# Optimization experiments

Hardware: AMD Instinct MI355X
Metric: run time of the kernel (lower is better)

Reference implementation:

```python
import jax, jax.numpy as jnp
import numpy as np

B, C, DET, T = 16, 1, 512, 180  # batch, channels, detector size (= image side, circle=True), n angles


def setup_inputs() -> dict:
    key = jax.random.key(0)
    x = jax.random.normal(key, (B, C, DET, T), dtype=jnp.float32)  # sinogram [B,C,det,theta]
    return {"x": x}


def _ramp_filter(x):
    """skimage-style ramp (Ram-Lak) filter along detector axis (axis=2)."""
    det = x.shape[2]
    size = max(64, int(2 ** np.ceil(np.log2(2 * det))))  # zero-padded FFT length
    n = np.concatenate([np.arange(1, size // 2 + 1, 2), np.arange(size // 2 - 1, 0, -2)])
    f = np.zeros(size, dtype=np.float64)
    f[0] = 0.25
    f[1::2] = -1.0 / (np.pi * n) ** 2
    fourier = (2.0 * np.real(np.fft.fft(f))).astype(np.float32)  # [size]
    xp = jnp.pad(x, ((0, 0), (0, 0), (0, size - det), (0, 0)))
    proj = jnp.fft.fft(xp, axis=2) * fourier[None, None, :, None]
    return jnp.real(jnp.fft.ifft(proj, axis=2))[:, :, :det, :].astype(x.dtype)


def _forward(x):
    b, c, det, n_theta = x.shape
    xf = _ramp_filter(x)
    # align_corners=False unit grid over the image (circle=True -> grid side == det)
    u = ((2.0 * jnp.arange(det, dtype=x.dtype) + 1.0) / det - 1.0)
    yg = u[:, None]  # [det,1] (meshgrid 'ij': Y varies over rows)
    xg = u[None, :]  # [1,det]
    rad = jnp.arange(n_theta, dtype=x.dtype) * jnp.asarray(np.pi / 180.0, x.dtype)
    cos_t, sin_t = jnp.cos(rad), jnp.sin(rad)

    # Note: the grid X coord theta_x[i]=(2i+1)/T-1 maps (align_corners=False) to pixel
    # index exactly i, so the width-axis bilinear interp reduces to taking angle column i.
    def body(reco, inp):
        i, c_, s_ = inp
        col = jax.lax.dynamic_index_in_dim(xf, i, axis=3, keepdims=False)  # [B,C,det]
        t = xg * c_ - yg * s_                      # [det,det] rotated coordinate
        iy = ((t + 1.0) * det - 1.0) / 2.0         # grid_sample align_corners=False
        i0f = jnp.floor(iy)
        w1 = iy - i0f
        w0 = 1.0 - w1
        i0 = i0f.astype(jnp.int32)
        i1 = i0 + 1
        m0 = ((i0 >= 0) & (i0 < det)).astype(xf.dtype)  # zeros padding
        m1 = ((i1 >= 0) & (i1 < det)).astype(xf.dtype)
        g0 = jnp.take(col, jnp.clip(i0, 0, det - 1), axis=2)  # [B,C,det,det]
        g1 = jnp.take(col, jnp.clip(i1, 0, det - 1), axis=2)
        return reco + (w0 * m0) * g0 + (w1 * m1) * g1, None

    reco0 = jnp.zeros((b, c, det, det), xf.dtype)
    reco, _ = jax.lax.scan(body, reco0, (jnp.arange(n_theta), cos_t, sin_t))

    # reconstruction circle mask (scikit=False -> radius^2 <= 1 - 1/in_size)
    mask = (xg ** 2 + yg ** 2) <= (1.0 - 1.0 / det)
    reco = jnp.where(mask[None, None], reco, jnp.zeros((), reco.dtype))
    return reco * jnp.asarray(np.pi / (2.0 * n_theta), reco.dtype)


def reference(x):
    return _forward(x)
```

## Files before the change

### kernel.cpp

```cpp
#include <hip/hip_runtime.h>
#include <math.h>

#define DET 512
#define NB  16
#define NT  180
#define PI_D 3.14159265358979323846
#define NPAIR 89
#define PADQ 108
#define NGP  45
#define PKI_ROW 1536
#define NOFF 101
#define NMRG 6
#define NBX  108

#define TT_OFF   8192
#define XF0_OFF  (TT_OFF + 512*512*2)
#define XF90_OFF (XF0_OFF + 32768)
#define PK_OFF   (XF90_OFF + 32768)

typedef _Float16 half8  __attribute__((ext_vector_type(8)));
typedef _Float16 half4v __attribute__((ext_vector_type(4)));
typedef _Float16 half2v __attribute__((ext_vector_type(2)));
typedef float    float4v __attribute__((ext_vector_type(4)));

__device__ inline void fmix_lo(float& acc, float w, unsigned int pk) {
  asm("v_fma_mix_f32 %0, %1, %2, %0 op_sel_hi:[0,1,0]"
      : "+v"(acc) : "v"(w), "v"(pk));
}
__device__ inline void fmix_hi(float& acc, float w, unsigned int pk) {
  asm("v_fma_mix_f32 %0, %1, %2, %0 op_sel:[0,1,0] op_sel_hi:[0,1,0]"
      : "+v"(acc) : "v"(w), "v"(pk));
}

__global__ __launch_bounds__(256) void filter_kernel(const float* __restrict__ x,
                                                     char* __restrict__ wsb) {
  __shared__ _Float16 xs_h[16][512];
  __shared__ _Float16 xs_l[16][512];
  __shared__ float xfs[16][65];
  __shared__ _Float16 wls[8][1032];
  unsigned int* pkg = (unsigned int*)(wsb + PK_OFF);

  int tid = threadIdx.x;
  int p = blockIdx.x, b = blockIdx.y;
  int dt0 = blockIdx.z * 2;

  {
    int k0 = tid * 4;
    const float CSC = (float)(-2048.0 / (PI_D * PI_D));
#pragma unroll
    for (int r = 0; r < 8; r++) {
      half4v v;
#pragma unroll
      for (int j = 0; j < 4; j++) {
        int delta = 511 - (k0 + j) - r;
        float wv;
        if (delta == 0) wv = 512.0f;
        else if (delta & 1) wv = CSC / (float)(delta * delta);
        else wv = 0.0f;
        v[j] = (_Float16)wv;
      }
      *(half4v*)&wls[r][k0] = v;
    }
  }

  int m = tid & 15, kp = tid >> 4;
  int tS;
  if (p < 11) tS = (m < 8) ? (8 * p + 1 + m) : (164 - 8 * p + m);
  else        tS = (m == 0) ? 89 : ((m == 1) ? 91 : ((m == 3) ? 90 : 0));
  const float* xb = x + (size_t)b * DET * NT + tS;
#pragma unroll 8
  for (int pass = 0; pass < 16; pass++) {
    int k = pass * 32 + kp * 2;
    int c = k >> 3, h = k & 7;
    int phys = (((c ^ (m & 7)) << 3) | h);
    float v0 = xb[(size_t)k * NT];
    float v1 = xb[(size_t)(k + 1) * NT];
    _Float16 h0 = (_Float16)v0, h1 = (_Float16)v1;
    half2v hh = {h0, h1};
    half2v ll = {(_Float16)(v0 - (float)h0), (_Float16)(v1 - (float)h1)};
    *(half2v*)&xs_h[m][phys] = hh;
    *(half2v*)&xs_l[m][phys] = ll;
  }
  __syncthreads();

  int nprb = (p < 11) ? 8 : 1;
  int tpb0 = (p < 11) ? 8 * p : 88;
  if (blockIdx.z == 0) {
    int idx = (tid < 108) ? tid : (620 + (tid - 108));
    uint2 z2; z2.x = 0u; z2.y = 0u;
    for (int pr = 0; pr < nprb; pr++) {
      int tq = (p < 11) ? (tpb0 + pr) : 88;
      int gp = (tq <= 44) ? tq : 88 - tq;
      *(uint2*)&pkg[((size_t)b * NGP + gp) * PKI_ROW + 2 * idx] = z2;
    }
  }

  int lane = tid & 63, wv = tid >> 6;
  int mm = lane & 15, q = lane >> 4;
  const _Float16* arh = &xs_h[mm][0];
  const _Float16* arl = &xs_l[mm][0];
  int e = mm & 7;
  int mp = tid >> 5, cc = (tid & 31) * 2;
  int rT = (p < 11) ? mp : 0;
  int rU = (p < 11) ? (15 - mp) : 1;
  int tpp = (p < 11) ? (8 * p + mp) : 88;
  bool dopack = (p < 11) || (mp == 0);
  int gp_  = (tpp <= 44) ? tpp : 88 - tpp;
  int slot = (tpp <= 44) ? 0 : 1;

  for (int dti = 0; dti < 2; dti++) {
    int dt = dt0 + dti;
    int dw = dt * 64 + wv * 16 + mm;
    int sdw = 511 - dw;
    const _Float16* thl = &wls[sdw & 7][sdw & ~7];
    float4v acc0 = {0.f, 0.f, 0.f, 0.f};
    float4v acc1 = {0.f, 0.f, 0.f, 0.f};
#pragma unroll 4
    for (int kc = 0; kc < 512; kc += 32) {
      int ph = ((((kc >> 3) + q) ^ e) << 3);
      half8 Ah = *(const half8*)&arh[ph];
      half8 Al = *(const half8*)&arl[ph];
      half8 Bh = *(const half8*)&thl[kc + q * 8];
      acc0 = __builtin_amdgcn_mfma_f32_16x16x32_f16(Ah, Bh, acc0, 0, 0, 0);
      acc1 = __builtin_amdgcn_mfma_f32_16x16x32_f16(Al, Bh, acc1, 0, 0, 0);
    }
    if (dti > 0) __syncthreads();
#pragma unroll
    for (int i = 0; i < 4; i++)
      xfs[q * 4 + i][wv * 16 + mm] = (acc0[i] + acc1[i]) * 0.0009765625f;
    __syncthreads();
    if (dopack) {
      float ft0 = xfs[rT][cc], ft1 = xfs[rT][cc + 1];
      float fu0 = xfs[rU][cc], fu1 = xfs[rU][cc + 1];
      auto p0 = __builtin_amdgcn_cvt_pkrtz(ft0, fu0);
      auto p1 = __builtin_amdgcn_cvt_pkrtz(ft1, fu1);
      unsigned int w0, w1;
      __builtin_memcpy(&w0, &p0, 4);
      __builtin_memcpy(&w1, &p1, 4);
      unsigned int* row = pkg + ((size_t)b * NGP + gp_) * PKI_ROW;
      int en = PADQ + dt * 64 + cc;
      row[2 * en + slot]     = w0;
      row[2 * en + 2 + slot] = w1;
      if (tpp == 44) {
        row[2 * en + 1] = w0;
        row[2 * en + 3] = w1;
      }
    }
    if (p == 11 && tid < 64) {
      float* f0  = (float*)(wsb + XF0_OFF)  + (size_t)b * DET;
      float* f90 = (float*)(wsb + XF90_OFF) + (size_t)b * DET;
      f0[dt * 64 + tid]  = xfs[2][tid];
      f90[dt * 64 + tid] = xfs[3][tid];
    }
  }
}


#define PROCESS(c_, s_, SW)                                                    \
  {                                                                            \
    float inner = fmaf(-(s_), q_, 363.5f);                                     \
    float iyA = fmaf( (c_), p_, inner);                                        \
    float iyB = fmaf(-(c_), p_, inner);                                        \
    int   iA = (int)iyA;  float wA = __builtin_amdgcn_fractf(iyA);             \
    int   iB = (int)iyB;  float wB = __builtin_amdgcn_fractf(iyB);             \
    float vA = 1.f - wA, vB = 1.f - wB;                                        \
    uint4 rA, rB, rMA, rMB;                                                    \
    __builtin_memcpy(&rA,  &colI[2 * iA], 16);                                 \
    __builtin_memcpy(&rB,  &colI[2 * iB], 16);                                 \
    __builtin_memcpy(&rMA, &colI[2 * (726 - iA)], 16);                         \
    __builtin_memcpy(&rMB, &colI[2 * (726 - iB)], 16);                         \
    unsigned tA0 = SW ? rA.y : rA.x,  tA1 = SW ? rA.w : rA.z;                  \
    unsigned uA0 = SW ? rA.x : rA.y,  uA1 = SW ? rA.z : rA.w;                  \
    unsigned tB0 = SW ? rB.y : rB.x,  tB1 = SW ? rB.w : rB.z;                  \
    unsigned uB0 = SW ? rB.x : rB.y,  uB1 = SW ? rB.z : rB.w;                  \
    unsigned tMA0 = SW ? rMA.y : rMA.x,  tMA1 = SW ? rMA.w : rMA.z;            \
    unsigned uMA0 = SW ? rMA.x : rMA.y,  uMA1 = SW ? rMA.z : rMA.w;            \
    unsigned tMB0 = SW ? rMB.y : rMB.x,  tMB1 = SW ? rMB.w : rMB.z;            \
    unsigned uMB0 = SW ? rMB.x : rMB.y,  uMB1 = SW ? rMB.z : rMB.w;            \
    fmix_lo(A1, vA, tA0);  fmix_lo(A1, wA, tA1);                               \
    fmix_hi(A1, vB, tB0);  fmix_hi(A1, wB, tB1);                               \
    fmix_lo(A2, vB, tB0);  fmix_lo(A2, wB, tB1);                               \
    fmix_hi(A2, vA, tA0);  fmix_hi(A2, wA, tA1);                               \
    fmix_lo(A3, wA, tMA0); fmix_lo(A3, vA, tMA1);                              \
    fmix_hi(A3, wB, tMB0); fmix_hi(A3, vB, tMB1);                              \
    fmix_lo(A4, wB, tMB0); fmix_lo(A4, vB, tMB1);                              \
    fmix_hi(A4, wA, tMA0); fmix_hi(A4, vA, tMA1);                              \
    fmix_lo(B1, wA, uMA0); fmix_lo(B1, vA, uMA1);                              \
    fmix_hi(B1, vB, uB0);  fmix_hi(B1, wB, uB1);                               \
    fmix_lo(B2, wB, uMB0); fmix_lo(B2, vB, uMB1);                              \
    fmix_hi(B2, vA, uA0);  fmix_hi(B2, wA, uA1);                               \
    fmix_lo(B3, vA, uA0);  fmix_lo(B3, wA, uA1);                               \
    fmix_hi(B3, wB, uMB0); fmix_hi(B3, vB, uMB1);                              \
    fmix_lo(B4, vB, uB0);  fmix_lo(B4, wB, uB1);                               \
    fmix_hi(B4, wA, uMA0); fmix_hi(B4, vA, uMA1);                              \
  }

#define PROCESSP(c_, s_, SW, pp, qq, AA1, AA2, AA3, AA4)                       \
  {                                                                            \
    float inner = fmaf(-(s_), (qq), 363.5f);                                   \
    float iyA = fmaf( (c_), (pp), inner);                                      \
    float iyB = fmaf(-(c_), (pp), inner);                                      \
    int   iA = (int)iyA;  float wA = __builtin_amdgcn_fractf(iyA);             \
    int   iB = (int)iyB;  float wB = __builtin_amdgcn_fractf(iyB);             \
    float vA = 1.f - wA, vB = 1.f - wB;                                        \
    uint4 rA, rB, rMA, rMB;                                                    \
    __builtin_memcpy(&rA,  &colI[2 * iA], 16);                                 \
    __builtin_memcpy(&rB,  &colI[2 * iB], 16);                                 \
    __builtin_memcpy(&rMA, &colI[2 * (726 - iA)], 16);                         \
    __builtin_memcpy(&rMB, &colI[2 * (726 - iB)], 16);                         \
    unsigned tA0 = SW ? rA.y : rA.x,  tA1 = SW ? rA.w : rA.z;                  \
    unsigned tB0 = SW ? rB.y : rB.x,  tB1 = SW ? rB.w : rB.z;                  \
    unsigned tMA0 = SW ? rMA.y : rMA.x,  tMA1 = SW ? rMA.w : rMA.z;            \
    unsigned tMB0 = SW ? rMB.y : rMB.x,  tMB1 = SW ? rMB.w : rMB.z;            \
    fmix_lo(AA1, vA, tA0);  fmix_lo(AA1, wA, tA1);                             \
    fmix_hi(AA1, vB, tB0);  fmix_hi(AA1, wB, tB1);                             \
    fmix_lo(AA2, vB, tB0);  fmix_lo(AA2, wB, tB1);                             \
    fmix_hi(AA2, vA, tA0);  fmix_hi(AA2, wA, tA1);                             \
    fmix_lo(AA3, wA, tMA0); fmix_lo(AA3, vA, tMA1);                            \
    fmix_hi(AA3, wB, tMB0); fmix_hi(AA3, vB, tMB1);                            \
    fmix_lo(AA4, wB, tMB0); fmix_lo(AA4, vB, tMB1);                            \
    fmix_hi(AA4, wA, tMA0); fmix_hi(AA4, vA, tMA1);                            \
  }

__global__ __launch_bounds__(256, 8) void backproj_kernel(
    const char* __restrict__ wsb, float* __restrict__ out) {
  __shared__ unsigned int pk[2][PKI_ROW];
  __shared__ float2 trigs[48];
  int tid = threadIdx.x;
  int b   = blockIdx.y;
  int bx  = blockIdx.x;
  int lx = tid & 15, ly = tid >> 4;
  float* ob = out + (size_t)b * DET * DET;
  int w = tid >> 6, l = tid & 63;

  if (bx == NOFF + NMRG) {
    const int LDEAD[10] = {10,8,6,5,4,3,2,2,1,1};
    for (int a = 0; a < 10; a++)
      for (int bt = 0; bt < LDEAD[a]; bt++) {
        int X1 = 16*a + lx, X2 = 511 - X1;
        int Y1 = 16*bt + ly, Y2 = 511 - Y1;
        ob[(size_t)Y1*DET + X1] = 0.f;
        ob[(size_t)Y1*DET + X2] = 0.f;
        ob[(size_t)Y2*DET + X1] = 0.f;
        ob[(size_t)Y2*DET + X2] = 0.f;
      }
    return;
  }

  if (tid < NGP) {
    float th = (float)(tid + 1) * (float)(PI_D / 180.0);
    float2 cs; cs.x = cosf(th); cs.y = sinf(th);
    trigs[tid] = cs;
  }

  const unsigned int* pkg = (const unsigned int*)(wsb + PK_OFF) + (size_t)b * NGP * PKI_ROW;

  auto stage_group = [&](int g, int par) {
    {
      const unsigned int* src = pkg + (size_t)g * PKI_ROW + w * 256 + l * 4;
      char* dst = (char*)&pk[par][0] + w * 1024;
      __builtin_amdgcn_global_load_lds(
          (const __attribute__((address_space(1))) unsigned int*)src,
          (__attribute__((address_space(3))) unsigned int*)dst, 16, 0, 0);
    }
    if (w < 2) {
      const unsigned int* src = pkg + (size_t)g * PKI_ROW + (w + 4) * 256 + l * 4;
      char* dst = (char*)&pk[par][0] + (w + 4) * 1024;
      __builtin_amdgcn_global_load_lds(
          (const __attribute__((address_space(1))) unsigned int*)src,
          (__attribute__((address_space(3))) unsigned int*)dst, 16, 0, 0);
    }
  };

  const float* f0  = (const float*)(wsb + XF0_OFF)  + (size_t)b * DET;
  const float* f90 = (const float*)(wsb + XF90_OFF) + (size_t)b * DET;
  const float SC = (float)(PI_D / 360.0);

  if (bx >= NOFF) {
    int d = bx - NOFF;
    int a1 = 4 + 2 * d, a2 = 5 + 2 * d;
    float p1_ = (float)(16 * a1 + lx) - 255.5f, q1_ = (float)(16 * a1 + ly) - 255.5f;
    float p2_ = (float)(16 * a2 + lx) - 255.5f, q2_ = (float)(16 * a2 + ly) - 255.5f;
    int mk1 = 481 - 32 * a1, mn1 = 505 - 32 * a1 - 8 * w;
    int mk2 = 481 - 32 * a2, mn2 = 505 - 32 * a2 - 8 * w;
    bool wl1 = (mk1 * mk1 + mn1 * mn1 <= 261632);
    bool wl2 = (mk2 * mk2 + mn2 * mn2 <= 261632);

    float A1=0.f, A2=0.f, A3=0.f, A4=0.f;
    float C1=0.f, C2=0.f, C3=0.f, C4=0.f;

    stage_group(0, 0);
    __syncthreads();
    for (int g = 0; g < NGP; g++) {
      if (g + 1 < NGP) stage_group(g + 1, (g + 1) & 1);
      float2 cs = trigs[g];
      const unsigned int* colI = &pk[g & 1][0];
      if (wl1) {
        PROCESSP(cs.x, cs.y, 0, p1_, q1_, A1, A2, A3, A4);
        if (g != 44) PROCESSP(cs.y, cs.x, 1, p1_, q1_, A1, A2, A3, A4);
      }
      if (wl2) {
        PROCESSP(cs.x, cs.y, 0, p2_, q2_, C1, C2, C3, C4);
        if (g != 44) PROCESSP(cs.y, cs.x, 1, p2_, q2_, C1, C2, C3, C4);
      }
      __syncthreads();
    }
#pragma unroll
    for (int t = 0; t < 2; t++) {
      int a = t ? a2 : a1;
      int X1 = 16 * a + lx, X2 = 511 - X1;
      int Y1 = 16 * a + ly, Y2 = 511 - Y1;
      int kx = 2 * X1 - 511, ky = 2 * Y1 - 511;
      bool in = (kx * kx + ky * ky) <= 261632;
      float g0x1 = f0[X1], g0x2 = f0[X2];
      float g90y1 = f90[Y1], g90y2 = f90[Y2];
      float P1 = (t ? C1 : A1) + g0x1 + g90y2;
      float P2 = (t ? C2 : A2) + g0x2 + g90y2;
      float P3 = (t ? C3 : A3) + g0x2 + g90y1;
      float P4 = (t ? C4 : A4) + g0x1 + g90y1;
      ob[(size_t)Y1 * DET + X1] = in ? P1 * SC : 0.f;
      ob[(size_t)Y1 * DET + X2] = in ? P2 * SC : 0.f;
      ob[(size_t)Y2 * DET + X2] = in ? P3 * SC : 0.f;
      ob[(size_t)Y2 * DET + X1] = in ? P4 * SC : 0.f;
    }
    return;
  }

  int a = (bx>=6)+(bx>=14)+(bx>=24)+(bx>=35)+(bx>=46)+(bx>=56)+(bx>=65)
        + (bx>=73)+(bx>=80)+(bx>=86)+(bx>=91)+(bx>=95)+(bx>=98)+(bx>=100);
  int Sa, bs;
  if (a < 8) { Sa = (int)((0x41382E23180E0600ULL >> (8*a)) & 0xFF);
               bs = (int)((0x080706050506080AULL >> (8*a)) & 0xFF); }
  else       { Sa = (int)((0x0064625F5B565049ULL >> (8*(a-8))) & 0xFF);
               bs = (int)((0x000F0E0D0C0B0A09ULL >> (8*(a-8))) & 0xFF); }
  int bt = bx - Sa + bs;
  int tx = 16*a, ty = 16*bt;

  int X1 = tx + lx, X2 = 511 - X1;
  int Y1 = ty + ly, Y2 = 511 - Y1;
  float p_ = (float)X1 - 255.5f;
  float q_ = (float)Y1 - 255.5f;

  int mkx = 481 - 32*a;
  int mky = 505 - 32*bt - 8*w;
  bool wlive = (mkx*mkx + mky*mky <= 261632);

  float A1=0.f, A2=0.f, A3=0.f, A4=0.f;
  float B1=0.f, B2=0.f, B3=0.f, B4=0.f;

  stage_group(0, 0);
  __syncthreads();

  for (int g = 0; g < NGP; g++) {
    if (g + 1 < NGP) stage_group(g + 1, (g + 1) & 1);
    float2 cs = trigs[g];
    const unsigned int* colI = &pk[g & 1][0];
    if (wlive) {
      PROCESS(cs.x, cs.y, 0);
      if (g != 44) PROCESS(cs.y, cs.x, 1);
    }
    __syncthreads();
  }

  int kx = 2*X1 - 511, ky = 2*Y1 - 511;
  bool in = (kx*kx + ky*ky) <= 261632;

  float g0x1 = f0[X1], g0x2 = f0[X2];
  float g90y1 = f90[Y1], g90y2 = f90[Y2];
  float P1 = A1 + g0x1 + g90y2;
  float P2 = A2 + g0x2 + g90y2;
  float P3 = A3 + g0x2 + g90y1;
  float P4 = A4 + g0x1 + g90y1;
  ob[(size_t)Y1*DET + X1] = in ? P1*SC : 0.f;
  ob[(size_t)Y1*DET + X2] = in ? P2*SC : 0.f;
  ob[(size_t)Y2*DET + X2] = in ? P3*SC : 0.f;
  ob[(size_t)Y2*DET + X1] = in ? P4*SC : 0.f;

  {
    float g0y1 = f0[Y1], g0y2 = f0[Y2];
    float g90x1 = f90[X1], g90x2 = f90[X2];
    float Q1 = B1 + g0y1 + g90x2;
    float Q2 = B2 + g0y1 + g90x1;
    float Q3 = B3 + g0y2 + g90x1;
    float Q4 = B4 + g0y2 + g90x2;
    Q1 = in ? Q1*SC : 0.f;
    Q2 = in ? Q2*SC : 0.f;
    Q3 = in ? Q3*SC : 0.f;
    Q4 = in ? Q4*SC : 0.f;
    __syncthreads();
    float* qs = (float*)&pk[0][0];
    qs[(0*16 + lx)*17 + ly] = Q1;
    qs[(1*16 + lx)*17 + ly] = Q2;
    qs[(2*16 + lx)*17 + ly] = Q3;
    qs[(3*16 + lx)*17 + ly] = Q4;
    __syncthreads();
    float o1 = qs[(0*16 + ly)*17 + lx];
    float o2 = qs[(1*16 + ly)*17 + lx];
    float o3 = qs[(2*16 + ly)*17 + lx];
    float o4 = qs[(3*16 + ly)*17 + lx];
    int r1 = tx + ly, r2 = 511 - r1;
    int c1 = ty + lx, c2 = 511 - c1;
    ob[(size_t)r1*DET + c1] = o1;
    ob[(size_t)r2*DET + c1] = o2;
    ob[(size_t)r2*DET + c2] = o3;
    ob[(size_t)r1*DET + c2] = o4;
  }
}

extern "C" void kernel_launch(void* const* d_in, const int* in_sizes, int n_in,
                              void* d_out, int out_size, void* d_ws, size_t ws_size,
                              hipStream_t stream) {
  (void)in_sizes; (void)n_in; (void)out_size; (void)ws_size;
  const float* x = (const float*)d_in[0];
  float* out = (float*)d_out;
  char*  wsb = (char*)d_ws;

  filter_kernel<<<dim3(12, 16, 4), 256, 0, stream>>>(x, wsb);
  backproj_kernel<<<dim3(NBX, NB), 256, 0, stream>>>(wsb, out);
}
```

Before: 139.2 us.

## Repack filtered projections as 16-byte entries and use fdot2 interpolation

The packed sinogram layout changes so each 16-byte entry already holds both neighbouring detector samples (i0 and i0+1) for the two paired angles. The backprojection can then fetch one uint4 per lookup and do each bilinear interpolation with a single packed-half fdot2 instead of two fma_mix ops. Weights are packed into half2 via cvt_pkrtz, which lowers weight precision to fp16. The change also doubles the LDS staging buffer, lowers the launch-bounds occupancy hint from 8 to 6, and flattens the grid with batch-interleaved block indexing. The filter kernel now writes duplicated half values with scattered 2-byte stores, which adds write traffic.

```diff
diff --git a/kernel.cpp b/kernel.cpp
--- a/kernel.cpp
+++ b/kernel.cpp
@@ -8,7 +8,8 @@
 #define NPAIR 89
 #define PADQ 108
 #define NGP  45
-#define PKI_ROW 1536
+#define NENT 768
+#define ROWB 12288
 #define NOFF 101
 #define NMRG 6
 #define NBX  108
@@ -23,13 +24,13 @@
 typedef _Float16 half2v __attribute__((ext_vector_type(2)));
 typedef float    float4v __attribute__((ext_vector_type(4)));
 
-__device__ inline void fmix_lo(float& acc, float w, unsigned int pk) {
-  asm("v_fma_mix_f32 %0, %1, %2, %0 op_sel_hi:[0,1,0]"
-      : "+v"(acc) : "v"(w), "v"(pk));
+__device__ inline half2v H2(unsigned u) { half2v h; __builtin_memcpy(&h, &u, 4); return h; }
+__device__ inline half2v pkrtz(float a, float b) {
+  auto r = __builtin_amdgcn_cvt_pkrtz(a, b);
+  half2v h; __builtin_memcpy(&h, &r, 4); return h;
 }
-__device__ inline void fmix_hi(float& acc, float w, unsigned int pk) {
-  asm("v_fma_mix_f32 %0, %1, %2, %0 op_sel:[0,1,0] op_sel_hi:[0,1,0]"
-      : "+v"(acc) : "v"(w), "v"(pk));
+__device__ inline float fdot2f(half2v a, half2v b, float c) {
+  return __builtin_amdgcn_fdot2(a, b, c, false);
 }
 
 __global__ __launch_bounds__(256) void filter_kernel(const float* __restrict__ x,
@@ -38,7 +39,7 @@
   __shared__ _Float16 xs_l[16][512];
   __shared__ float xfs[16][65];
   __shared__ _Float16 wls[8][1032];
-  unsigned int* pkg = (unsigned int*)(wsb + PK_OFF);
+  char* pkb = wsb + PK_OFF;
 
   int tid = threadIdx.x;
   int p = blockIdx.x, b = blockIdx.y;
@@ -86,12 +87,23 @@
   int nprb = (p < 11) ? 8 : 1;
   int tpb0 = (p < 11) ? 8 * p : 88;
   if (blockIdx.z == 0) {
-    int idx = (tid < 108) ? tid : (620 + (tid - 108));
-    uint2 z2; z2.x = 0u; z2.y = 0u;
     for (int pr = 0; pr < nprb; pr++) {
       int tq = (p < 11) ? (tpb0 + pr) : 88;
       int gp = (tq <= 44) ? tq : 88 - tq;
-      *(uint2*)&pkg[((size_t)b * NGP + gp) * PKI_ROW + 2 * idx] = z2;
+      char* base = pkb + ((size_t)b * NGP + gp) * ROWB;
+      if (tid < 107) {
+        uint4 z4 = {0u, 0u, 0u, 0u};
+        *(uint4*)(base + (size_t)tid * 16) = z4;
+      } else if (tid < 255) {
+        uint4 z4 = {0u, 0u, 0u, 0u};
+        *(uint4*)(base + (size_t)(620 + tid - 107) * 16) = z4;
+      } else {
+        unsigned short z = 0;
+        *(unsigned short*)(base + 107*16 + 0)  = z; *(unsigned short*)(base + 107*16 + 4)  = z;
+        *(unsigned short*)(base + 107*16 + 8)  = z; *(unsigned short*)(base + 107*16 + 12) = z;
+        *(unsigned short*)(base + 619*16 + 2)  = z; *(unsigned short*)(base + 619*16 + 6)  = z;
+        *(unsigned short*)(base + 619*16 + 10) = z; *(unsigned short*)(base + 619*16 + 14) = z;
+      }
     }
   }
 
@@ -106,7 +118,7 @@
   int tpp = (p < 11) ? (8 * p + mp) : 88;
   bool dopack = (p < 11) || (mp == 0);
   int gp_  = (tpp <= 44) ? tpp : 88 - tpp;
-  int slot = (tpp <= 44) ? 0 : 1;
+  int so   = (tpp <= 44) ? 0 : 8;
 
   for (int dti = 0; dti < 2; dti++) {
     int dt = dt0 + dti;
@@ -130,20 +142,23 @@
       xfs[q * 4 + i][wv * 16 + mm] = (acc0[i] + acc1[i]) * 0.0009765625f;
     __syncthreads();
     if (dopack) {
-      float ft0 = xfs[rT][cc], ft1 = xfs[rT][cc + 1];
-      float fu0 = xfs[rU][cc], fu1 = xfs[rU][cc + 1];
-      auto p0 = __builtin_amdgcn_cvt_pkrtz(ft0, fu0);
-      auto p1 = __builtin_amdgcn_cvt_pkrtz(ft1, fu1);
-      unsigned int w0, w1;
-      __builtin_memcpy(&w0, &p0, 4);
-      __builtin_memcpy(&w1, &p1, 4);
-      unsigned int* row = pkg + ((size_t)b * NGP + gp_) * PKI_ROW;
-      int en = PADQ + dt * 64 + cc;
-      row[2 * en + slot]     = w0;
-      row[2 * en + 2 + slot] = w1;
-      if (tpp == 44) {
-        row[2 * en + 1] = w0;
-        row[2 * en + 3] = w1;
+      char* base = pkb + ((size_t)b * NGP + gp_) * ROWB;
+#pragma unroll
+      for (int ci = 0; ci < 2; ci++) {
+        int c = cc + ci;
+        _Float16 ftc = (_Float16)xfs[rT][c];
+        _Float16 fuc = (_Float16)xfs[rU][c];
+        int en = PADQ + dt * 64 + c;
+        *(_Float16*)(base + (size_t)en * 16 + 0 + so)       = ftc;
+        *(_Float16*)(base + (size_t)(en - 1) * 16 + 2 + so) = ftc;
+        *(_Float16*)(base + (size_t)en * 16 + 4 + so)       = fuc;
+        *(_Float16*)(base + (size_t)(en - 1) * 16 + 6 + so) = fuc;
+        if (tpp == 44) {
+          *(_Float16*)(base + (size_t)en * 16 + 8)        = ftc;
+          *(_Float16*)(base + (size_t)(en - 1) * 16 + 10) = ftc;
+          *(_Float16*)(base + (size_t)en * 16 + 12)       = fuc;
+          *(_Float16*)(base + (size_t)(en - 1) * 16 + 14) = fuc;
+        }
       }
     }
     if (p == 11 && tid < 64) {
@@ -155,6 +170,9 @@
   }
 }
 
+#define XTRACT(nm, qq, SW)                                                     \
+  half2v Tft##nm = H2(SW ? qq.z : qq.x), Tfu##nm = H2(SW ? qq.w : qq.y);       \
+  half2v Uft##nm = H2(SW ? qq.x : qq.z), Ufu##nm = H2(SW ? qq.y : qq.w);
 
 #define PROCESS(c_, s_, SW)                                                    \
   {                                                                            \
@@ -163,77 +181,61 @@
     float iyB = fmaf(-(c_), p_, inner);                                        \
     int   iA = (int)iyA;  float wA = __builtin_amdgcn_fractf(iyA);             \
     int   iB = (int)iyB;  float wB = __builtin_amdgcn_fractf(iyB);             \
-    float vA = 1.f - wA, vB = 1.f - wB;                                        \
-    uint4 rA, rB, rMA, rMB;                                                    \
-    __builtin_memcpy(&rA,  &colI[2 * iA], 16);                                 \
-    __builtin_memcpy(&rB,  &colI[2 * iB], 16);                                 \
-    __builtin_memcpy(&rMA, &colI[2 * (726 - iA)], 16);                         \
-    __builtin_memcpy(&rMB, &colI[2 * (726 - iB)], 16);                         \
-    unsigned tA0 = SW ? rA.y : rA.x,  tA1 = SW ? rA.w : rA.z;                  \
-    unsigned uA0 = SW ? rA.x : rA.y,  uA1 = SW ? rA.z : rA.w;                  \
-    unsigned tB0 = SW ? rB.y : rB.x,  tB1 = SW ? rB.w : rB.z;                  \
-    unsigned uB0 = SW ? rB.x : rB.y,  uB1 = SW ? rB.z : rB.w;                  \
-    unsigned tMA0 = SW ? rMA.y : rMA.x,  tMA1 = SW ? rMA.w : rMA.z;            \
-    unsigned uMA0 = SW ? rMA.x : rMA.y,  uMA1 = SW ? rMA.z : rMA.w;            \
-    unsigned tMB0 = SW ? rMB.y : rMB.x,  tMB1 = SW ? rMB.w : rMB.z;            \
-    unsigned uMB0 = SW ? rMB.x : rMB.y,  uMB1 = SW ? rMB.z : rMB.w;            \
-    fmix_lo(A1, vA, tA0);  fmix_lo(A1, wA, tA1);                               \
-    fmix_hi(A1, vB, tB0);  fmix_hi(A1, wB, tB1);                               \
-    fmix_lo(A2, vB, tB0);  fmix_lo(A2, wB, tB1);                               \
-    fmix_hi(A2, vA, tA0);  fmix_hi(A2, wA, tA1);                               \
-    fmix_lo(A3, wA, tMA0); fmix_lo(A3, vA, tMA1);                              \
-    fmix_hi(A3, wB, tMB0); fmix_hi(A3, vB, tMB1);                              \
-    fmix_lo(A4, wB, tMB0); fmix_lo(A4, vB, tMB1);                              \
-    fmix_hi(A4, wA, tMA0); fmix_hi(A4, vA, tMA1);                              \
-    fmix_lo(B1, wA, uMA0); fmix_lo(B1, vA, uMA1);                              \
-    fmix_hi(B1, vB, uB0);  fmix_hi(B1, wB, uB1);                               \
-    fmix_lo(B2, wB, uMB0); fmix_lo(B2, vB, uMB1);                              \
-    fmix_hi(B2, vA, uA0);  fmix_hi(B2, wA, uA1);                               \
-    fmix_lo(B3, vA, uA0);  fmix_lo(B3, wA, uA1);                               \
-    fmix_hi(B3, wB, uMB0); fmix_hi(B3, vB, uMB1);                              \
-    fmix_lo(B4, vB, uB0);  fmix_lo(B4, wB, uB1);                               \
-    fmix_hi(B4, wA, uMA0); fmix_hi(B4, vA, uMA1);                              \
-  }
-
-#define PROCESSP(c_, s_, SW, pp, qq, AA1, AA2, AA3, AA4)                       \
+    half2v wpA = pkrtz(1.f - wA, wA);                                          \
+    half2v wpAr = pkrtz(wA, 1.f - wA);                                         \
+    half2v wpB = pkrtz(1.f - wB, wB);                                          \
+    half2v wpBr = pkrtz(wB, 1.f - wB);                                         \
+    uint4 qA = colI[iA], qB = colI[iB];                                        \
+    uint4 qMA = colI[726 - iA], qMB = colI[726 - iB];                          \
+    XTRACT(A, qA, SW)  XTRACT(B, qB, SW)                                       \
+    XTRACT(MA, qMA, SW) XTRACT(MB, qMB, SW)                                    \
+    A1 = fdot2f(wpA, TftA, A1);   A1 = fdot2f(wpB, TfuB, A1);                  \
+    A2 = fdot2f(wpB, TftB, A2);   A2 = fdot2f(wpA, TfuA, A2);                  \
+    A3 = fdot2f(wpAr, TftMA, A3); A3 = fdot2f(wpBr, TfuMB, A3);                \
+    A4 = fdot2f(wpBr, TftMB, A4); A4 = fdot2f(wpAr, TfuMA, A4);                \
+    B1 = fdot2f(wpAr, UftMA, B1); B1 = fdot2f(wpB, UfuB, B1);                  \
+    B2 = fdot2f(wpBr, UftMB, B2); B2 = fdot2f(wpA, UfuA, B2);                  \
+    B3 = fdot2f(wpA, UftA, B3);   B3 = fdot2f(wpBr, UfuMB, B3);                \
+    B4 = fdot2f(wpB, UftB, B4);   B4 = fdot2f(wpAr, UfuMA, B4);                \
+  }
+
+#define PROCESSP(c_, s_, SW, pp, qq_, AA1, AA2, AA3, AA4)                      \
   {                                                                            \
-    float inner = fmaf(-(s_), (qq), 363.5f);                                   \
+    float inner = fmaf(-(s_), (qq_), 363.5f);                                  \
     float iyA = fmaf( (c_), (pp), inner);                                      \
     float iyB = fmaf(-(c_), (pp), inner);                                      \
     int   iA = (int)iyA;  float wA = __builtin_amdgcn_fractf(iyA);             \
     int   iB = (int)iyB;  float wB = __builtin_amdgcn_fractf(iyB);             \
-    float vA = 1.f - wA, vB = 1.f - wB;                                        \
-    uint4 rA, rB, rMA, rMB;                                                    \
-    __builtin_memcpy(&rA,  &colI[2 * iA], 16);                                 \
-    __builtin_memcpy(&rB,  &colI[2 * iB], 16);                                 \
-    __builtin_memcpy(&rMA, &colI[2 * (726 - iA)], 16);                         \
-    __builtin_memcpy(&rMB, &colI[2 * (726 - iB)], 16);                         \
-    unsigned tA0 = SW ? rA.y : rA.x,  tA1 = SW ? rA.w : rA.z;                  \
-    unsigned tB0 = SW ? rB.y : rB.x,  tB1 = SW ? rB.w : rB.z;                  \
-    unsigned tMA0 = SW ? rMA.y : rMA.x,  tMA1 = SW ? rMA.w : rMA.z;            \
-    unsigned tMB0 = SW ? rMB.y : rMB.x,  tMB1 = SW ? rMB.w : rMB.z;            \
-    fmix_lo(AA1, vA, tA0);  fmix_lo(AA1, wA, tA1);                             \
-    fmix_hi(AA1, vB, tB0);  fmix_hi(AA1, wB, tB1);                             \
-    fmix_lo(AA2, vB, tB0);  fmix_lo(AA2, wB, tB1);                             \
-    fmix_hi(AA2, vA, tA0);  fmix_hi(AA2, wA, tA1);                             \
-    fmix_lo(AA3, wA, tMA0); fmix_lo(AA3, vA, tMA1);                            \
-    fmix_hi(AA3, wB, tMB0); fmix_hi(AA3, vB, tMB1);                            \
-    fmix_lo(AA4, wB, tMB0); fmix_lo(AA4, vB, tMB1);                            \
-    fmix_hi(AA4, wA, tMA0); fmix_hi(AA4, vA, tMA1);                            \
-  }
-
-__global__ __launch_bounds__(256, 8) void backproj_kernel(
+    half2v wpA = pkrtz(1.f - wA, wA);                                          \
+    half2v wpAr = pkrtz(wA, 1.f - wA);                                         \
+    half2v wpB = pkrtz(1.f - wB, wB);                                          \
+    half2v wpBr = pkrtz(wB, 1.f - wB);                                         \
+    uint4 qA = colI[iA], qB = colI[iB];                                        \
+    uint4 qMA = colI[726 - iA], qMB = colI[726 - iB];                          \
+    half2v TftA = H2(SW ? qA.z : qA.x),  TfuA = H2(SW ? qA.w : qA.y);          \
+    half2v TftB = H2(SW ? qB.z : qB.x),  TfuB = H2(SW ? qB.w : qB.y);          \
+    half2v TftMA = H2(SW ? qMA.z : qMA.x), TfuMA = H2(SW ? qMA.w : qMA.y);     \
+    half2v TftMB = H2(SW ? qMB.z : qMB.x), TfuMB = H2(SW ? qMB.w : qMB.y);     \
+    AA1 = fdot2f(wpA, TftA, AA1);   AA1 = fdot2f(wpB, TfuB, AA1);              \
+    AA2 = fdot2f(wpB, TftB, AA2);   AA2 = fdot2f(wpA, TfuA, AA2);              \
+    AA3 = fdot2f(wpAr, TftMA, AA3); AA3 = fdot2f(wpBr, TfuMB, AA3);            \
+    AA4 = fdot2f(wpBr, TftMB, AA4); AA4 = fdot2f(wpAr, TfuMA, AA4);            \
+  }
+
+__global__ __launch_bounds__(256, 6) void backproj_kernel(
     const char* __restrict__ wsb, float* __restrict__ out) {
-  __shared__ unsigned int pk[2][PKI_ROW];
+  __shared__ uint4 pk[2][NENT];
   __shared__ float2 trigs[48];
   int tid = threadIdx.x;
-  int b   = blockIdx.y;
-  int bx  = blockIdx.x;
+  int f = blockIdx.x;
+  int sub = f & 15;
+  int b = 2 * (sub & 7) + (sub >> 3);
+  int bx = f >> 4;
   int lx = tid & 15, ly = tid >> 4;
   float* ob = out + (size_t)b * DET * DET;
   int w = tid >> 6, l = tid & 63;
 
-  if (bx == NOFF + NMRG) {
+  if (bx == NBX - 1) {
     const int LDEAD[10] = {10,8,6,5,4,3,2,2,1,1};
     for (int a = 0; a < 10; a++)
       for (int bt = 0; bt < LDEAD[a]; bt++) {
@@ -253,19 +255,14 @@
     trigs[tid] = cs;
   }
 
-  const unsigned int* pkg = (const unsigned int*)(wsb + PK_OFF) + (size_t)b * NGP * PKI_ROW;
+  const char* pkgb = wsb + PK_OFF + (size_t)b * NGP * ROWB;
 
   auto stage_group = [&](int g, int par) {
-    {
-      const unsigned int* src = pkg + (size_t)g * PKI_ROW + w * 256 + l * 4;
-      char* dst = (char*)&pk[par][0] + w * 1024;
-      __builtin_amdgcn_global_load_lds(
-          (const __attribute__((address_space(1))) unsigned int*)src,
-          (__attribute__((address_space(3))) unsigned int*)dst, 16, 0, 0);
-    }
-    if (w < 2) {
-      const unsigned int* src = pkg + (size_t)g * PKI_ROW + (w + 4) * 256 + l * 4;
-      char* dst = (char*)&pk[par][0] + (w + 4) * 1024;
+#pragma unroll
+    for (int i = 0; i < 3; i++) {
+      int c = w + 4 * i;
+      const char* src = pkgb + (size_t)g * ROWB + c * 1024 + l * 16;
+      char* dst = (char*)&pk[par][0] + c * 1024;
       __builtin_amdgcn_global_load_lds(
           (const __attribute__((address_space(1))) unsigned int*)src,
           (__attribute__((address_space(3))) unsigned int*)dst, 16, 0, 0);
@@ -294,7 +291,7 @@
     for (int g = 0; g < NGP; g++) {
       if (g + 1 < NGP) stage_group(g + 1, (g + 1) & 1);
       float2 cs = trigs[g];
-      const unsigned int* colI = &pk[g & 1][0];
+      const uint4* colI = &pk[g & 1][0];
       if (wl1) {
         PROCESSP(cs.x, cs.y, 0, p1_, q1_, A1, A2, A3, A4);
         if (g != 44) PROCESSP(cs.y, cs.x, 1, p1_, q1_, A1, A2, A3, A4);
@@ -354,7 +351,7 @@
   for (int g = 0; g < NGP; g++) {
     if (g + 1 < NGP) stage_group(g + 1, (g + 1) & 1);
     float2 cs = trigs[g];
-    const unsigned int* colI = &pk[g & 1][0];
+    const uint4* colI = &pk[g & 1][0];
     if (wlive) {
       PROCESS(cs.x, cs.y, 0);
       if (g != 44) PROCESS(cs.y, cs.x, 1);
@@ -416,5 +413,5 @@
   char*  wsb = (char*)d_ws;
 
   filter_kernel<<<dim3(12, 16, 4), 256, 0, stream>>>(x, wsb);
-  backproj_kernel<<<dim3(NBX, NB), 256, 0, stream>>>(wsb, out);
+  backproj_kernel<<<dim3(NBX * NB), 256, 0, stream>>>(wsb, out);
 }
```

Measured after the change: 146.1 us. +4.9%, slower.
